# Kernel tuning notes

Measured on AMD Instinct MI355X. Metric: run time of the kernel, lower is better.

The kernel has to match this reference:

```python
import jax, jax.numpy as jnp
import numpy as np
from jax import lax

T, B, D, H, K, A = 256, 512, 128, 50, 5, 4


def setup_inputs() -> dict:
    key = jax.random.key(0)
    ks = jax.random.split(key, 12)
    s = 0.05
    return {
        "x": jax.random.normal(ks[0], (T, B, D), dtype=jnp.float32),
        "W_in": jax.random.normal(ks[1], (H, D), dtype=jnp.float32) * s,
        "b_in": jax.random.normal(ks[2], (H,), dtype=jnp.float32) * s,
        "W_ctx": jax.random.normal(ks[3], (H, 2 * H), dtype=jnp.float32) * s,
        "b_ctx": jax.random.normal(ks[4], (H,), dtype=jnp.float32) * s,
        "W_key": jax.random.normal(ks[5], (K, H), dtype=jnp.float32) * s,
        "b_key": jax.random.normal(ks[6], (K,), dtype=jnp.float32) * s,
        "W_q": jax.random.normal(ks[7], (K, H), dtype=jnp.float32) * s,
        "b_q": jax.random.normal(ks[8], (K,), dtype=jnp.float32) * s,
        "first_context": jax.random.normal(ks[9], (H,), dtype=jnp.float32) * s,
        "W_act": jax.random.normal(ks[10], (A, H), dtype=jnp.float32) * s,
        "b_act": jax.random.normal(ks[11], (A,), dtype=jnp.float32) * s,
    }


def reference(x, W_in, b_in, W_ctx, b_ctx, W_key, b_key, W_q, b_q,
              first_context, W_act, b_act):
    # Unrolls the torch module's per-step forward() over T steps with a
    # growing attention context (horizon=-1 => attend to full history).
    Tn, Bn, _ = x.shape
    Hn = W_in.shape[0]
    Kn = W_key.shape[0]
    neg_inf = jnp.float32(-1e30)

    c0 = jnp.broadcast_to(first_context[None, :], (Bn, Hn))  # [B,H]
    ctx_buf = jnp.zeros((Tn + 1, Bn, Hn), x.dtype).at[0].set(c0)
    key_buf = jnp.zeros((Tn + 1, Bn, Kn), x.dtype).at[0].set(c0 @ W_key.T + b_key)
    step_ids = jnp.arange(Tn + 1)[:, None]  # [T+1,1]

    def step(carry, xt):
        ctx_buf, key_buf, prev_c, t = carry
        h = jax.nn.relu(xt @ W_in.T + b_in)                           # [B,H]
        c = jax.nn.relu(jnp.concatenate([prev_c, h], axis=1) @ W_ctx.T + b_ctx)
        ctx_buf = ctx_buf.at[t + 1].set(c)
        key_buf = key_buf.at[t + 1].set(c @ W_key.T + b_key)
        q = c @ W_q.T + b_q                                           # [B,K]
        scores = jnp.einsum('tbk,bk->tb', key_buf, q)                 # [T+1,B]
        scores = jnp.where(step_ids <= t + 1, scores, neg_inf)
        attn = jax.nn.softmax(scores, axis=0)                         # over history
        w = jnp.einsum('tb,tbh->bh', attn, ctx_buf)                   # [B,H]
        actions = w @ W_act.T + b_act                                 # [B,A]
        return (ctx_buf, key_buf, c, t + 1), actions

    _, actions = lax.scan(step, (ctx_buf, key_buf, c0, jnp.int32(0)), x)
    return actions  # [T,B,A]
```

## Files before the change

### kernel.cpp

```cpp
#include <hip/hip_runtime.h>

#define TT 256
#define BB 512
#define DD 128
#define HH 50
#define KK 5
#define AA 4
#define NROW 131072
#define GST 52
#define CXS 66
#define KQR2 18

#define R50(X) X(0) X(1) X(2) X(3) X(4) X(5) X(6) X(7) X(8) X(9) \
  X(10) X(11) X(12) X(13) X(14) X(15) X(16) X(17) X(18) X(19) \
  X(20) X(21) X(22) X(23) X(24) X(25) X(26) X(27) X(28) X(29) \
  X(30) X(31) X(32) X(33) X(34) X(35) X(36) X(37) X(38) X(39) \
  X(40) X(41) X(42) X(43) X(44) X(45) X(46) X(47) X(48) X(49)

typedef _Float16 half4 __attribute__((ext_vector_type(4)));
typedef float f32x4 __attribute__((ext_vector_type(4)));

__global__ void k0_prep(const float* __restrict__ W_in,
                        const float* __restrict__ W_ctx,
                        const float* __restrict__ W_key,
                        const float* __restrict__ W_q,
                        const float* __restrict__ b_key,
                        const float* __restrict__ b_q,
                        float* __restrict__ WHT,
                        float* __restrict__ WK2T, float* __restrict__ bias2) {
  int i = blockIdx.x * 256 + threadIdx.x;
  if (i < HH * 52) {
    int j = i / 52, h = i % 52;
    WHT[i] = (h < HH) ? W_ctx[h * (2 * HH) + HH + j] : 0.f;
  }
  if (i < HH * 64) {
    int j = i >> 6, l = i & 63;
    float v = 0.f;
    if (l < HH) v = W_ctx[l * (2 * HH) + j];
    else if (l < HH + KK) v = W_key[(l - HH) * HH + j];
    else if (l < HH + 2 * KK) v = W_q[(l - HH - KK) * HH + j];
    WK2T[i] = v;
  }
  if (i < 64) {
    float bv = 0.f;
    if (i >= HH && i < HH + KK) bv = b_key[i - HH];
    else if (i >= HH + KK && i < HH + 2 * KK) bv = b_q[i - HH - KK];
    bias2[i] = bv;
  }
}

__global__ __launch_bounds__(256, 2) void k1_mfma(
    const float* __restrict__ x, const float* __restrict__ W_in,
    const float* __restrict__ WHT, const float* __restrict__ b_in,
    const float* __restrict__ b_ctx, float* __restrict__ g) {
  const int lane = threadIdx.x & 63;
  const int wave = threadIdx.x >> 6;
  const int lrow = lane & 15, lgrp = lane >> 4;

#define WA1D(m, kk)                                                     \
  half4 wa1_##m##_##kk;                                                 \
  {                                                                     \
    const int hh = 16 * (m) + lrow;                                     \
    const int j0 = 16 * (kk) + 4 * lgrp;                                \
    const bool v = (hh < HH);                                           \
    const float* p = W_in + (size_t)(v ? hh : 0) * DD + j0;             \
    wa1_##m##_##kk[0] = (_Float16)(v ? p[0] : 0.f);                     \
    wa1_##m##_##kk[1] = (_Float16)(v ? p[1] : 0.f);                     \
    wa1_##m##_##kk[2] = (_Float16)(v ? p[2] : 0.f);                     \
    wa1_##m##_##kk[3] = (_Float16)(v ? p[3] : 0.f);                     \
  }
  WA1D(0, 0) WA1D(0, 1) WA1D(0, 2) WA1D(0, 3)
  WA1D(0, 4) WA1D(0, 5) WA1D(0, 6) WA1D(0, 7)
  WA1D(1, 0) WA1D(1, 1) WA1D(1, 2) WA1D(1, 3)
  WA1D(1, 4) WA1D(1, 5) WA1D(1, 6) WA1D(1, 7)
  WA1D(2, 0) WA1D(2, 1) WA1D(2, 2) WA1D(2, 3)
  WA1D(2, 4) WA1D(2, 5) WA1D(2, 6) WA1D(2, 7)
  WA1D(3, 0) WA1D(3, 1) WA1D(3, 2) WA1D(3, 3)
  WA1D(3, 4) WA1D(3, 5) WA1D(3, 6) WA1D(3, 7)

#define WA2D(m, kk)                                                     \
  half4 wa2_##m##_##kk;                                                 \
  {                                                                     \
    const int gg = 16 * (m) + lrow;                                     \
    const int h0 = 16 * (kk) + 4 * lgrp;                                \
    wa2_##m##_##kk[0] = (_Float16)((gg < HH && h0 + 0 < HH) ? WHT[(h0 + 0) * 52 + gg] : 0.f); \
    wa2_##m##_##kk[1] = (_Float16)((gg < HH && h0 + 1 < HH) ? WHT[(h0 + 1) * 52 + gg] : 0.f); \
    wa2_##m##_##kk[2] = (_Float16)((gg < HH && h0 + 2 < HH) ? WHT[(h0 + 2) * 52 + gg] : 0.f); \
    wa2_##m##_##kk[3] = (_Float16)((gg < HH && h0 + 3 < HH) ? WHT[(h0 + 3) * 52 + gg] : 0.f); \
  }
  WA2D(0, 0) WA2D(0, 1) WA2D(0, 2) WA2D(0, 3)
  WA2D(1, 0) WA2D(1, 1) WA2D(1, 2) WA2D(1, 3)
  WA2D(2, 0) WA2D(2, 1) WA2D(2, 2) WA2D(2, 3)
  WA2D(3, 0) WA2D(3, 1) WA2D(3, 2) WA2D(3, 3)

#define BDEF(m, r)                                                      \
  const float bin_##m##_##r =                                           \
      (16 * (m) + 4 * lgrp + (r) < HH) ? b_in[16 * (m) + 4 * lgrp + (r)] : 0.f; \
  const float bct_##m##_##r =                                           \
      (16 * (m) + 4 * lgrp + (r) < HH) ? b_ctx[16 * (m) + 4 * lgrp + (r)] : 0.f;
  BDEF(0, 0) BDEF(0, 1) BDEF(0, 2) BDEF(0, 3)
  BDEF(1, 0) BDEF(1, 1) BDEF(1, 2) BDEF(1, 3)
  BDEF(2, 0) BDEF(2, 1) BDEF(2, 2) BDEF(2, 3)
  BDEF(3, 0) BDEF(3, 1) BDEF(3, 2) BDEF(3, 3)

  const f32x4 zf = {0.f, 0.f, 0.f, 0.f};

#pragma unroll 1
  for (int it = 0; it < 4; ++it) {
    const int tile = (blockIdx.x * 4 + wave) * 4 + it;
    const int row = tile * 16 + lrow;
    const float* __restrict__ xr = x + (size_t)row * DD + 4 * lgrp;

#define XLD(kk)                                                         \
  half4 xb##kk;                                                         \
  {                                                                     \
    const float4 xv = *reinterpret_cast<const float4*>(xr + 16 * kk);   \
    xb##kk[0] = (_Float16)xv.x;                                         \
    xb##kk[1] = (_Float16)xv.y;                                         \
    xb##kk[2] = (_Float16)xv.z;                                         \
    xb##kk[3] = (_Float16)xv.w;                                         \
  }
    XLD(0) XLD(1) XLD(2) XLD(3) XLD(4) XLD(5) XLD(6) XLD(7)

    f32x4 d10 = zf, d11 = zf, d12 = zf, d13 = zf;
#define MM1(kk)                                                              \
  d10 = __builtin_amdgcn_mfma_f32_16x16x16f16(wa1_0_##kk, xb##kk, d10, 0, 0, 0); \
  d11 = __builtin_amdgcn_mfma_f32_16x16x16f16(wa1_1_##kk, xb##kk, d11, 0, 0, 0); \
  d12 = __builtin_amdgcn_mfma_f32_16x16x16f16(wa1_2_##kk, xb##kk, d12, 0, 0, 0); \
  d13 = __builtin_amdgcn_mfma_f32_16x16x16f16(wa1_3_##kk, xb##kk, d13, 0, 0, 0);
    MM1(0) MM1(1) MM1(2) MM1(3) MM1(4) MM1(5) MM1(6) MM1(7)

#define HBD(k)                                                    \
  half4 hb##k;                                                    \
  hb##k[0] = (_Float16)fmaxf(d1##k[0] + bin_##k##_0, 0.f);        \
  hb##k[1] = (_Float16)fmaxf(d1##k[1] + bin_##k##_1, 0.f);        \
  hb##k[2] = (_Float16)fmaxf(d1##k[2] + bin_##k##_2, 0.f);        \
  hb##k[3] = (_Float16)fmaxf(d1##k[3] + bin_##k##_3, 0.f);
    HBD(0) HBD(1) HBD(2) HBD(3)

    f32x4 d20 = zf, d21 = zf, d22 = zf, d23 = zf;
#define MM2(kk)                                                              \
  d20 = __builtin_amdgcn_mfma_f32_16x16x16f16(wa2_0_##kk, hb##kk, d20, 0, 0, 0); \
  d21 = __builtin_amdgcn_mfma_f32_16x16x16f16(wa2_1_##kk, hb##kk, d21, 0, 0, 0); \
  d22 = __builtin_amdgcn_mfma_f32_16x16x16f16(wa2_2_##kk, hb##kk, d22, 0, 0, 0); \
  d23 = __builtin_amdgcn_mfma_f32_16x16x16f16(wa2_3_##kk, hb##kk, d23, 0, 0, 0);
    MM2(0) MM2(1) MM2(2) MM2(3)

    float* __restrict__ gr =
        g + ((size_t)(row & (BB - 1)) * TT + (row >> 9)) * GST;
    *reinterpret_cast<float4*>(gr + 4 * lgrp) =
        make_float4(d20[0] + bct_0_0, d20[1] + bct_0_1, d20[2] + bct_0_2,
                    d20[3] + bct_0_3);
    *reinterpret_cast<float4*>(gr + 16 + 4 * lgrp) =
        make_float4(d21[0] + bct_1_0, d21[1] + bct_1_1, d21[2] + bct_1_2,
                    d21[3] + bct_1_3);
    *reinterpret_cast<float4*>(gr + 32 + 4 * lgrp) =
        make_float4(d22[0] + bct_2_0, d22[1] + bct_2_1, d22[2] + bct_2_2,
                    d22[3] + bct_2_3);
    if (lgrp == 0) {
      *reinterpret_cast<float4*>(gr + 48) =
          make_float4(d23[0] + bct_3_0, d23[1] + bct_3_1, 0.f, 0.f);
    }
  }
}

__global__ __launch_bounds__(256, 2) void k23_fused(
    const float* __restrict__ g, const float* __restrict__ WK2T,
    const float* __restrict__ bias2, const float* __restrict__ fc,
    const float* __restrict__ W_act, const float* __restrict__ b_act,
    float* __restrict__ out) {
  __shared__ _Float16 ctx_l[272 * CXS];
  __shared__ _Float16 kq_l[272 * KQR2];
  __shared__ __align__(16) float c_lds[64];
  __shared__ int prog;

  const int tid = threadIdx.x;
  const int b = blockIdx.x;
  const int wv = tid >> 6;
  const int lane = tid & 63;

  for (int i = tid; i < 272 * CXS; i += 256) ctx_l[i] = (_Float16)0.f;
  for (int i = tid; i < 272 * KQR2; i += 256) kq_l[i] = (_Float16)0.f;
  if (tid == 0) prog = 0;
  __syncthreads();

  if (wv == 0) {
    __builtin_amdgcn_s_setprio(3);
#define WDECL(j)                            \
  float w##j = WK2T[(j) * 64 + lane];       \
  asm volatile("" : "+v"(w##j));
    R50(WDECL)
    const float wz = 0.f;
    const float bias = bias2[lane];

    const float c0v = (lane < HH) ? fc[lane] : 0.f;
    c_lds[lane] = (lane < HH) ? c0v : 0.f;
    if (lane < HH) ctx_l[0 * CXS + lane] = (_Float16)c0v;

    const int gslot = (lane < GST) ? lane : (GST - 1);
    const float* __restrict__ gbp = g + (size_t)b * TT * GST + gslot;
    float gq0 = gbp[0 * GST];
    float gq1 = gbp[1 * GST];
    float gq2 = gbp[2 * GST];
    float gq3 = gbp[3 * GST];

#define KQ(J, wa, wb, wc, wd)                                            \
  {                                                                      \
    const float4 cq = *reinterpret_cast<const float4*>(&c_lds[J]);       \
    acc0 = fmaf(wa, cq.x, acc0);                                         \
    acc1 = fmaf(wb, cq.y, acc1);                                         \
    acc2 = fmaf(wc, cq.z, acc2);                                         \
    acc3 = fmaf(wd, cq.w, acc3);                                         \
  }
#define DOT50R                                                           \
  float acc0 = 0.f, acc1 = 0.f, acc2 = 0.f, acc3 = 0.f;                  \
  KQ(0, w0, w1, w2, w3) KQ(4, w4, w5, w6, w7)                            \
  KQ(8, w8, w9, w10, w11) KQ(12, w12, w13, w14, w15)                     \
  KQ(16, w16, w17, w18, w19) KQ(20, w20, w21, w22, w23)                  \
  KQ(24, w24, w25, w26, w27) KQ(28, w28, w29, w30, w31)                  \
  KQ(32, w32, w33, w34, w35) KQ(36, w36, w37, w38, w39)                  \
  KQ(40, w40, w41, w42, w43) KQ(44, w44, w45, w46, w47)                  \
  KQ(48, w48, w49, wz, wz)                                               \
  const float acc = (acc0 + acc1) + (acc2 + acc3);

#define BODYF(RR, GQ)                                                    \
  {                                                                      \
    const int t = tg4 + RR;                                              \
    DOT50R                                                               \
    if (lane >= HH) kq_l[t * KQR2 + (lane - HH)] = (_Float16)(acc + bias); \
    const float cn = fmaxf(acc + GQ, 0.f);                               \
    GQ = gbp[(size_t)min(t + 4, TT - 1) * GST];                          \
    if (lane < HH) {                                                     \
      ctx_l[(t + 1) * CXS + lane] = (_Float16)cn;                        \
      c_lds[lane] = cn;                                                  \
    }                                                                    \
  }

#pragma unroll 1
    for (int tg4 = 0; tg4 < TT; tg4 += 4) {
      BODYF(0, gq0) BODYF(1, gq1) BODYF(2, gq2) BODYF(3, gq3)
      if (tg4 & 4) {
        asm volatile("" ::: "memory");
        if (lane == 0) *((volatile int*)&prog) = tg4 + 4;
      }
    }

    {
      DOT50R
      if (lane >= HH) kq_l[TT * KQR2 + (lane - HH)] = (_Float16)(acc + bias);
    }
    asm volatile("" ::: "memory");
    __builtin_amdgcn_s_setprio(0);
    if (lane == 0) *((volatile int*)&prog) = 257;

  } else {
    const int lrow = lane & 15, lgrp = lane >> 4;
    const f32x4 zf = {0.f, 0.f, 0.f, 0.f};

#define WACT(a, ht)                                                     \
  const float wa_##a##_##ht =                                           \
      (lrow + 16 * (ht) < HH) ? W_act[(a)*HH + lrow + 16 * (ht)] : 0.f;
    WACT(0, 0) WACT(0, 1) WACT(0, 2) WACT(0, 3)
    WACT(1, 0) WACT(1, 1) WACT(1, 2) WACT(1, 3)
    WACT(2, 0) WACT(2, 1) WACT(2, 2) WACT(2, 3)
    WACT(3, 0) WACT(3, 1) WACT(3, 2) WACT(3, 3)
    const float ba0 = b_act[0], ba1 = b_act[1];
    const float ba2 = b_act[2], ba3 = b_act[3];

#pragma unroll 1
    for (int k = wv - 1; k < 16; k += 3) {
      const int tw = k * 16;
      const int need = (tw + 17 > 257) ? 257 : (tw + 17);
      while (*((volatile int*)&prog) < need) __builtin_amdgcn_s_sleep(32);
      asm volatile("" ::: "memory");

      half4 qf;
#pragma unroll
      for (int i = 0; i < 4; ++i) {
        const int kk = 4 * lgrp + i;
        qf[i] = (kk < KK) ? kq_l[(tw + lrow + 1) * KQR2 + 5 + kk]
                          : (_Float16)0.f;
      }

      f32x4 oa0 = zf, oa1 = zf, oa2 = zf, oa3 = zf;
      float su = 0.f;

#pragma unroll 1
      for (int sb = 0; sb <= tw + 16; sb += 16) {
        half4 kf;
#pragma unroll
        for (int i = 0; i < 4; ++i)
          kf[i] = kq_l[(sb + lrow) * KQR2 + 4 * lgrp + i];

        const f32x4 sc =
            __builtin_amdgcn_mfma_f32_16x16x16f16(kf, qf, zf, 0, 0, 0);

        half4 pa;
#pragma unroll
        for (int r = 0; r < 4; ++r) {
          const int s = sb + 4 * lgrp + r;
          const float p = (s <= tw + lrow + 1) ? __expf(sc[r]) : 0.f;
          su += p;
          pa[r] = (_Float16)p;
        }

        const int vb = sb + 4 * lgrp;
#define PVF(HT, ACC)                                                      \
  {                                                                       \
    half4 vf;                                                             \
    vf[0] = ctx_l[(vb + 0) * CXS + lrow + 16 * HT];                       \
    vf[1] = ctx_l[(vb + 1) * CXS + lrow + 16 * HT];                       \
    vf[2] = ctx_l[(vb + 2) * CXS + lrow + 16 * HT];                       \
    vf[3] = ctx_l[(vb + 3) * CXS + lrow + 16 * HT];                       \
    ACC = __builtin_amdgcn_mfma_f32_16x16x16f16(pa, vf, ACC, 0, 0, 0);    \
  }
        PVF(0, oa0) PVF(1, oa1) PVF(2, oa2) PVF(3, oa3)
      }

      su += __shfl_xor(su, 16, 64);
      su += __shfl_xor(su, 32, 64);

#define PTC(r)                                                                 \
  float pt##r##_0 = oa0[r] * wa_0_0 + oa1[r] * wa_0_1 + oa2[r] * wa_0_2 +      \
                    oa3[r] * wa_0_3;                                           \
  float pt##r##_1 = oa0[r] * wa_1_0 + oa1[r] * wa_1_1 + oa2[r] * wa_1_2 +      \
                    oa3[r] * wa_1_3;                                           \
  float pt##r##_2 = oa0[r] * wa_2_0 + oa1[r] * wa_2_1 + oa2[r] * wa_2_2 +      \
                    oa3[r] * wa_2_3;                                           \
  float pt##r##_3 = oa0[r] * wa_3_0 + oa1[r] * wa_3_1 + oa2[r] * wa_3_2 +      \
                    oa3[r] * wa_3_3;
      PTC(0) PTC(1) PTC(2) PTC(3)
#define REDX(v)                 \
  v += __shfl_xor(v, 1, 64);    \
  v += __shfl_xor(v, 2, 64);    \
  v += __shfl_xor(v, 4, 64);    \
  v += __shfl_xor(v, 8, 64);
      REDX(pt0_0) REDX(pt0_1) REDX(pt0_2) REDX(pt0_3)
      REDX(pt1_0) REDX(pt1_1) REDX(pt1_2) REDX(pt1_3)
      REDX(pt2_0) REDX(pt2_1) REDX(pt2_2) REDX(pt2_3)
      REDX(pt3_0) REDX(pt3_1) REDX(pt3_2) REDX(pt3_3)

#define EPI(r)                                                            \
  {                                                                       \
    const float sur = __shfl(su, 4 * lgrp + (r), 64);                     \
    if (lrow == 0) {                                                      \
      const float inv = 1.f / sur;                                        \
      const int t = tw + 4 * lgrp + (r);                                  \
      *reinterpret_cast<float4*>(out + ((size_t)t * BB + b) * AA) =       \
          make_float4(fmaf(pt##r##_0, inv, ba0), fmaf(pt##r##_1, inv, ba1), \
                      fmaf(pt##r##_2, inv, ba2), fmaf(pt##r##_3, inv, ba3)); \
    }                                                                     \
  }
      EPI(0) EPI(1) EPI(2) EPI(3)
    }
  }
}

extern "C" void kernel_launch(void* const* d_in, const int* in_sizes, int n_in,
                              void* d_out, int out_size, void* d_ws,
                              size_t ws_size, hipStream_t stream) {
  const float* x = (const float*)d_in[0];
  const float* W_in = (const float*)d_in[1];
  const float* b_in = (const float*)d_in[2];
  const float* W_ctx = (const float*)d_in[3];
  const float* b_ctx = (const float*)d_in[4];
  const float* W_key = (const float*)d_in[5];
  const float* b_key = (const float*)d_in[6];
  const float* W_q = (const float*)d_in[7];
  const float* b_q = (const float*)d_in[8];
  const float* fc = (const float*)d_in[9];
  const float* W_act = (const float*)d_in[10];
  const float* b_act = (const float*)d_in[11];
  float* out = (float*)d_out;
  float* ws = (float*)d_ws;

  float* WHT = ws;
  float* WK2T = ws + 4096;
  float* bias2 = ws + 8128;
  float* g = ws + 8192;

  hipLaunchKernelGGL(k0_prep, dim3(26), dim3(256), 0, stream, W_in, W_ctx,
                     W_key, W_q, b_key, b_q, WHT, WK2T, bias2);
  hipLaunchKernelGGL(k1_mfma, dim3(512), dim3(256), 0, stream, x, W_in, WHT,
                     b_in, b_ctx, g);
  hipLaunchKernelGGL(k23_fused, dim3(512), dim3(256), 0, stream, g, WK2T,
                     bias2, fc, W_act, b_act, out);
}
```

Before: 142.4 us.

## Transpose context LDS buffer and pad key/query rows for vectorized half4 loads

The context history in shared memory is stored transposed (hidden-major, time contiguous) so each MFMA V-operand fragment becomes a single 8-byte half4 load instead of four scalar 2-byte loads. Key and query rows are restrided to 20 halfs with queries moved to an aligned offset, so the K and Q fragments also load as half4 vectors. This cuts LDS instruction count in the attention loop. In exchange the producer wave now does strided, possibly bank-conflicting scalar stores into the transposed buffer.

Result: no change. 140.7 us (-1.2%).

```diff
diff --git a/kernel.cpp b/kernel.cpp
--- a/kernel.cpp
+++ b/kernel.cpp
@@ -8,8 +8,8 @@
 #define AA 4
 #define NROW 131072
 #define GST 52
-#define CXS 66
-#define KQR2 18
+#define CXS2 276
+#define KQS2 20
 
 #define R50(X) X(0) X(1) X(2) X(3) X(4) X(5) X(6) X(7) X(8) X(9) \
   X(10) X(11) X(12) X(13) X(14) X(15) X(16) X(17) X(18) X(19) \
@@ -169,8 +169,8 @@
     const float* __restrict__ bias2, const float* __restrict__ fc,
     const float* __restrict__ W_act, const float* __restrict__ b_act,
     float* __restrict__ out) {
-  __shared__ _Float16 ctx_l[272 * CXS];
-  __shared__ _Float16 kq_l[272 * KQR2];
+  __shared__ _Float16 ctx_lT[64 * CXS2];
+  __shared__ _Float16 kq_l[272 * KQS2];
   __shared__ __align__(16) float c_lds[64];
   __shared__ int prog;
 
@@ -179,8 +179,8 @@
   const int wv = tid >> 6;
   const int lane = tid & 63;
 
-  for (int i = tid; i < 272 * CXS; i += 256) ctx_l[i] = (_Float16)0.f;
-  for (int i = tid; i < 272 * KQR2; i += 256) kq_l[i] = (_Float16)0.f;
+  for (int i = tid; i < 64 * CXS2; i += 256) ctx_lT[i] = (_Float16)0.f;
+  for (int i = tid; i < 272 * KQS2; i += 256) kq_l[i] = (_Float16)0.f;
   if (tid == 0) prog = 0;
   __syncthreads();
 
@@ -195,7 +195,7 @@
 
     const float c0v = (lane < HH) ? fc[lane] : 0.f;
     c_lds[lane] = (lane < HH) ? c0v : 0.f;
-    if (lane < HH) ctx_l[0 * CXS + lane] = (_Float16)c0v;
+    if (lane < HH) ctx_lT[lane * CXS2 + 0] = (_Float16)c0v;
 
     const int gslot = (lane < GST) ? lane : (GST - 1);
     const float* __restrict__ gbp = g + (size_t)b * TT * GST + gslot;
@@ -203,6 +203,10 @@
     float gq1 = gbp[1 * GST];
     float gq2 = gbp[2 * GST];
     float gq3 = gbp[3 * GST];
+
+    const bool iskq = (lane >= HH && lane < HH + 2 * KK);
+    const int kslot = iskq ? ((lane < HH + KK) ? lane - HH : lane - HH - KK + 8)
+                           : 0;
 
 #define KQ(J, wa, wb, wc, wd)                                            \
   {                                                                      \
@@ -227,11 +231,11 @@
   {                                                                      \
     const int t = tg4 + RR;                                              \
     DOT50R                                                               \
-    if (lane >= HH) kq_l[t * KQR2 + (lane - HH)] = (_Float16)(acc + bias); \
+    if (iskq) kq_l[t * KQS2 + kslot] = (_Float16)(acc + bias);           \
     const float cn = fmaxf(acc + GQ, 0.f);                               \
     GQ = gbp[(size_t)min(t + 4, TT - 1) * GST];                          \
     if (lane < HH) {                                                     \
-      ctx_l[(t + 1) * CXS + lane] = (_Float16)cn;                        \
+      ctx_lT[lane * CXS2 + (t + 1)] = (_Float16)cn;                      \
       c_lds[lane] = cn;                                                  \
     }                                                                    \
   }
@@ -247,7 +251,7 @@
 
     {
       DOT50R
-      if (lane >= HH) kq_l[TT * KQR2 + (lane - HH)] = (_Float16)(acc + bias);
+      if (iskq) kq_l[TT * KQS2 + kslot] = (_Float16)(acc + bias);
     }
     asm volatile("" ::: "memory");
     __builtin_amdgcn_s_setprio(0);
@@ -274,23 +278,18 @@
       while (*((volatile int*)&prog) < need) __builtin_amdgcn_s_sleep(32);
       asm volatile("" ::: "memory");
 
-      half4 qf;
-#pragma unroll
-      for (int i = 0; i < 4; ++i) {
-        const int kk = 4 * lgrp + i;
-        qf[i] = (kk < KK) ? kq_l[(tw + lrow + 1) * KQR2 + 5 + kk]
-                          : (_Float16)0.f;
-      }
+      half4 qf = {(_Float16)0.f, (_Float16)0.f, (_Float16)0.f, (_Float16)0.f};
+      if (lgrp < 3)
+        qf = *reinterpret_cast<const half4*>(
+            &kq_l[(tw + lrow + 1) * KQS2 + 8 + 4 * lgrp]);
 
       f32x4 oa0 = zf, oa1 = zf, oa2 = zf, oa3 = zf;
       float su = 0.f;
 
 #pragma unroll 1
       for (int sb = 0; sb <= tw + 16; sb += 16) {
-        half4 kf;
-#pragma unroll
-        for (int i = 0; i < 4; ++i)
-          kf[i] = kq_l[(sb + lrow) * KQR2 + 4 * lgrp + i];
+        const half4 kf = *reinterpret_cast<const half4*>(
+            &kq_l[(sb + lrow) * KQS2 + 4 * lgrp]);
 
         const f32x4 sc =
             __builtin_amdgcn_mfma_f32_16x16x16f16(kf, qf, zf, 0, 0, 0);
@@ -307,11 +306,8 @@
         const int vb = sb + 4 * lgrp;
 #define PVF(HT, ACC)                                                      \
   {                                                                       \
-    half4 vf;                                                             \
-    vf[0] = ctx_l[(vb + 0) * CXS + lrow + 16 * HT];                       \
-    vf[1] = ctx_l[(vb + 1) * CXS + lrow + 16 * HT];                       \
-    vf[2] = ctx_l[(vb + 2) * CXS + lrow + 16 * HT];                       \
-    vf[3] = ctx_l[(vb + 3) * CXS + lrow + 16 * HT];                       \
+    const half4 vf = *reinterpret_cast<const half4*>(                     \
+        &ctx_lT[(lrow + 16 * HT) * CXS2 + vb]);                           \
     ACC = __builtin_amdgcn_mfma_f32_16x16x16f16(pa, vf, ACC, 0, 0, 0);    \
   }
         PVF(0, oa0) PVF(1, oa1) PVF(2, oa2) PVF(3, oa3)
```
